# Kernel tuning notes

Hardware: AMD Instinct MI355X
Metric: run time of the kernel (lower is better)

## Reference

```python
import jax, jax.numpy as jnp
import numpy as np

NUM_HEADS = 16
HEAD_DIM = 64  # hidden_size 1024 / 16 heads


def setup_inputs() -> dict:
    key = jax.random.key(0)
    k1, k2, k3, k4 = jax.random.split(key, 4)
    B, S, Dm = 1, 2048, 1024
    scale = 1.0 / np.sqrt(Dm)
    return {
        "hidden_states": jax.random.normal(k1, (B, S, Dm), dtype=jnp.float32),
        "Wq": jax.random.normal(k2, (Dm, Dm), dtype=jnp.float32) * scale,
        "Wk": jax.random.normal(k3, (Dm, Dm), dtype=jnp.float32) * scale,
        "Wv": jax.random.normal(k4, (Dm, Dm), dtype=jnp.float32) * scale,
    }


def reference(hidden_states, Wq, Wk, Wv):
    # hidden_states: [B, S, Dm]; Wq/Wk/Wv: [Dm, Dm] (no bias)
    B, S, Dm = hidden_states.shape
    H, D = NUM_HEADS, HEAD_DIM
    q = (hidden_states @ Wq).reshape(B, S, H, D)
    k = (hidden_states @ Wk).reshape(B, S, H, D)
    v = (hidden_states @ Wv).reshape(B, S, H, D)
    # scaled dot-product scores: [B, H, Sq, Sk]
    scores = jnp.einsum("bqhd,bkhd->bhqk", q, k) / jnp.sqrt(jnp.float32(D))
    probs = jax.nn.softmax(scores, axis=-1)
    # context: [B, Sq, H, D] -> [B, Sq, H*D]
    context = jnp.einsum("bhqk,bkhd->bqhd", probs, v).reshape(B, S, H * D)
    # module permutes scores [B, Sq, Sk, H] -> [B, H, Sq, Sk]; we built that layout directly
    return context, probs
```

## Files before the change

### kernel.cpp

```cpp
#include <hip/hip_runtime.h>
#include <cstdint>
#include <cstddef>

#define SEQ 2048
#define DMODEL 1024
#define NHEADS 16
#define HDIM 64

typedef __attribute__((ext_vector_type(8))) short short8;
typedef __attribute__((ext_vector_type(4))) float floatx4;

__device__ __forceinline__ short f2bf(float f) {
  union { float f; uint32_t u; } x; x.f = f;
  uint32_t r = (x.u + 0x7FFFu + ((x.u >> 16) & 1u)) >> 16;
  return (short)(uint16_t)r;
}

__device__ __forceinline__ void gl_lds16(const short* g, short* l) {
  __builtin_amdgcn_global_load_lds((const __attribute__((address_space(1))) void*)g,
                                   (__attribute__((address_space(3))) void*)l, 16, 0, 0);
}

__global__ __launch_bounds__(256) void cast_bf16_kernel(const float* __restrict__ src,
                                                        short* __restrict__ dst, int n) {
  int i = blockIdx.x * 256 + threadIdx.x;
  if (i < n) dst[i] = f2bf(src[i]);
}

__global__ __launch_bounds__(256) void transpose_cast_kernel(const float* __restrict__ src,
                                                             short* __restrict__ dst) {
  __shared__ float tile[32][33];
  int tx = threadIdx.x, ty = threadIdx.y;
  int x = blockIdx.x * 32 + tx;
  int y0 = blockIdx.y * 32;
#pragma unroll
  for (int j = 0; j < 32; j += 8)
    tile[ty + j][tx] = src[(size_t)(y0 + ty + j) * DMODEL + x];
  __syncthreads();
  int xo = blockIdx.y * 32 + tx;
  int yo0 = blockIdx.x * 32;
#pragma unroll
  for (int j = 0; j < 32; j += 8)
    dst[(size_t)(yo0 + ty + j) * DMODEL + xo] = f2bf(tile[tx][ty + j]);
}

__global__ __launch_bounds__(256) void qkv_gemm_kernel(const short* __restrict__ Xb,
                                                       const short* __restrict__ Wt,
                                                       short* __restrict__ q,
                                                       short* __restrict__ k,
                                                       short* __restrict__ vT) {
  __shared__ short Ab[2][64 * 32];
  __shared__ short Bb[2][128 * 32];
  int tid = threadIdx.x;
  int wave = tid >> 6, lane = tid & 63;
  int lr = lane & 15, quad = lane >> 4;
  int m0 = blockIdx.y * 64;
  int n0 = blockIdx.x * 128;
  int wr = wave >> 1, wc = wave & 1;

  const short* Ag = Xb + (size_t)(m0 + (tid >> 2)) * DMODEL + (tid & 3) * 8;
  const short* Bg = Wt + (size_t)(n0 + (tid >> 2)) * DMODEL + (tid & 3) * 8;
  bool isV = (n0 >= 2 * DMODEL);

  floatx4 acc[2][4] = {};

  gl_lds16(Ag, Ab[0] + wave * 512);
  gl_lds16(Bg, Bb[0] + wave * 512);
  gl_lds16(Bg + 64 * DMODEL, Bb[0] + 2048 + wave * 512);
  __syncthreads();

  int cur = 0;
  for (int t = 0; t < 32; ++t) {
    if (t < 31) {
      int kb = (t + 1) * 32;
      gl_lds16(Ag + kb, Ab[cur ^ 1] + wave * 512);
      gl_lds16(Bg + kb, Bb[cur ^ 1] + wave * 512);
      gl_lds16(Bg + kb + 64 * DMODEL, Bb[cur ^ 1] + 2048 + wave * 512);
    }
    short8 a[2], b[4];
#pragma unroll
    for (int i = 0; i < 2; ++i)
      a[i] = *(const short8*)(Ab[cur] + (wr * 32 + i * 16 + lr) * 32 + quad * 8);
#pragma unroll
    for (int j = 0; j < 4; ++j)
      b[j] = *(const short8*)(Bb[cur] + (wc * 64 + j * 16 + lr) * 32 + quad * 8);
    if (isV) {
#pragma unroll
      for (int i = 0; i < 2; ++i)
#pragma unroll
        for (int j = 0; j < 4; ++j)
          acc[i][j] = __builtin_amdgcn_mfma_f32_16x16x32_bf16(b[j], a[i], acc[i][j], 0, 0, 0);
    } else {
#pragma unroll
      for (int i = 0; i < 2; ++i)
#pragma unroll
        for (int j = 0; j < 4; ++j)
          acc[i][j] = __builtin_amdgcn_mfma_f32_16x16x32_bf16(a[i], b[j], acc[i][j], 0, 0, 0);
    }
    __syncthreads();
    cur ^= 1;
  }

  if (!isV) {
    short* out = (n0 < DMODEL) ? q : k;
    int nbase = n0 & (DMODEL - 1);
#pragma unroll
    for (int i = 0; i < 2; ++i)
#pragma unroll
      for (int j = 0; j < 4; ++j) {
        int n = nbase + wc * 64 + j * 16 + lr;
        int hh = n >> 6, d = n & 63;
        size_t base = ((size_t)hh * SEQ + m0 + wr * 32 + i * 16 + quad * 4) * HDIM + d;
#pragma unroll
        for (int r = 0; r < 4; ++r) out[base + (size_t)r * HDIM] = f2bf(acc[i][j][r]);
      }
  } else {
    int nbase = n0 - 2 * DMODEL;
#pragma unroll
    for (int i = 0; i < 2; ++i) {
      int sidx = m0 + wr * 32 + i * 16 + lr;
#pragma unroll
      for (int j = 0; j < 4; ++j) {
        int n = nbase + wc * 64 + j * 16 + quad * 4;
#pragma unroll
        for (int r = 0; r < 4; ++r) vT[(size_t)(n + r) * SEQ + sidx] = f2bf(acc[i][j][r]);
      }
    }
  }
}

#define PSTRF 132

__global__ __launch_bounds__(256, 4) void attn_fused_kernel(const short* __restrict__ q,
                                                            const short* __restrict__ k,
                                                            const short* __restrict__ vT,
                                                            float* __restrict__ probs,
                                                            float* __restrict__ ctx) {
  __shared__ float pf[4][16 * PSTRF];
  __shared__ float wm[4][16], wl[4][16];

  int h = blockIdx.y;
  int m0 = blockIdx.x * 16;
  int wave = threadIdx.x >> 6, lane = threadIdx.x & 63;
  int lr = lane & 15, quad = lane >> 4;
  int nb = wave * 512;

  const short* Q = q + ((size_t)h * SEQ + m0 + lr) * HDIM + quad * 8;
  short8 qa0 = *(const short8*)(Q);
  short8 qa1 = *(const short8*)(Q + 32);
  const short* K = k + (size_t)h * SEQ * HDIM + quad * 8;

  float mrow[4], lrow[4];
#pragma unroll
  for (int r = 0; r < 4; ++r) { mrow[r] = -3.4e38f; lrow[r] = 0.f; }

#pragma unroll 1
  for (int c = 0; c < 4; ++c) {
    floatx4 s[8];
#pragma unroll
    for (int f = 0; f < 8; ++f) {
      const short* Kr = K + (size_t)(nb + c * 128 + f * 16 + lr) * HDIM;
      short8 b0 = *(const short8*)(Kr);
      short8 b1 = *(const short8*)(Kr + 32);
      floatx4 t = {};
      t = __builtin_amdgcn_mfma_f32_16x16x32_bf16(qa0, b0, t, 0, 0, 0);
      s[f] = __builtin_amdgcn_mfma_f32_16x16x32_bf16(qa1, b1, t, 0, 0, 0);
    }
#pragma unroll
    for (int r = 0; r < 4; ++r) {
      float cm = s[0][r];
#pragma unroll
      for (int f = 1; f < 8; ++f) cm = fmaxf(cm, s[f][r]);
      cm *= 0.125f;
      float mn = fmaxf(mrow[r], cm);
      float sum = 0.f;
#pragma unroll
      for (int f = 0; f < 8; ++f) sum += __expf(s[f][r] * 0.125f - mn);
      lrow[r] = lrow[r] * __expf(mrow[r] - mn) + sum;
      mrow[r] = mn;
    }
  }

#pragma unroll
  for (int off = 8; off >= 1; off >>= 1)
#pragma unroll
    for (int r = 0; r < 4; ++r) {
      float om = __shfl_xor(mrow[r], off);
      float ol = __shfl_xor(lrow[r], off);
      float mn = fmaxf(mrow[r], om);
      lrow[r] = lrow[r] * __expf(mrow[r] - mn) + ol * __expf(om - mn);
      mrow[r] = mn;
    }
  if (lr == 0)
#pragma unroll
    for (int r = 0; r < 4; ++r) {
      wm[wave][quad * 4 + r] = mrow[r];
      wl[wave][quad * 4 + r] = lrow[r];
    }
  __syncthreads();
  float inv[4];
#pragma unroll
  for (int r = 0; r < 4; ++r) {
    int row = quad * 4 + r;
    float m4 = fmaxf(fmaxf(wm[0][row], wm[1][row]), fmaxf(wm[2][row], wm[3][row]));
    float l4 = wl[0][row] * __expf(wm[0][row] - m4) + wl[1][row] * __expf(wm[1][row] - m4) +
               wl[2][row] * __expf(wm[2][row] - m4) + wl[3][row] * __expf(wm[3][row] - m4);
    mrow[r] = m4;
    inv[r] = 1.0f / l4;
  }

  float* pw = pf[wave];
  const short* Vb = vT + (size_t)h * HDIM * SEQ;
  floatx4 cacc[4] = {};
  int prow = lane >> 5;
  int pchunk = lane & 31;

#pragma unroll 1
  for (int c = 0; c < 4; ++c) {
    floatx4 s[8];
#pragma unroll
    for (int f = 0; f < 8; ++f) {
      const short* Kr = K + (size_t)(nb + c * 128 + f * 16 + lr) * HDIM;
      short8 b0 = *(const short8*)(Kr);
      short8 b1 = *(const short8*)(Kr + 32);
      floatx4 t = {};
      t = __builtin_amdgcn_mfma_f32_16x16x32_bf16(qa0, b0, t, 0, 0, 0);
      s[f] = __builtin_amdgcn_mfma_f32_16x16x32_bf16(qa1, b1, t, 0, 0, 0);
    }
#pragma unroll
    for (int f = 0; f < 8; ++f)
#pragma unroll
      for (int r = 0; r < 4; ++r)
        pw[(quad * 4 + r) * PSTRF + f * 16 + lr] = __expf(s[f][r] * 0.125f - mrow[r]) * inv[r];
#pragma unroll
    for (int i = 0; i < 8; ++i) {
      int row = i * 2 + prow;
      floatx4 v4 = *(const floatx4*)(pw + row * PSTRF + pchunk * 4);
      __builtin_nontemporal_store(
          v4, (floatx4*)(probs + ((size_t)h * SEQ + m0 + row) * SEQ + nb + c * 128 + pchunk * 4));
    }
#pragma unroll
    for (int kt = 0; kt < 128; kt += 32) {
      const float* pa = pw + lr * PSTRF + kt + quad * 8;
      floatx4 p0 = *(const floatx4*)(pa);
      floatx4 p1 = *(const floatx4*)(pa + 4);
      short8 a;
#pragma unroll
      for (int j = 0; j < 4; ++j) {
        a[j] = f2bf(p0[j]);
        a[4 + j] = f2bf(p1[j]);
      }
#pragma unroll
      for (int f = 0; f < 4; ++f) {
        short8 b = *(const short8*)(Vb + (size_t)(f * 16 + lr) * SEQ + nb + c * 128 + kt + quad * 8);
        cacc[f] = __builtin_amdgcn_mfma_f32_16x16x32_bf16(a, b, cacc[f], 0, 0, 0);
      }
    }
  }

  float* part = pf[wave];
#pragma unroll
  for (int f = 0; f < 4; ++f)
#pragma unroll
    for (int r = 0; r < 4; ++r) part[(quad * 4 + r) * 64 + f * 16 + lr] = cacc[f][r];
  __syncthreads();
  for (int e = threadIdx.x; e < 16 * 64; e += 256) {
    int m = e >> 6, d = e & 63;
    float v = pf[0][m * 64 + d] + pf[1][m * 64 + d] + pf[2][m * 64 + d] + pf[3][m * 64 + d];
    ctx[(size_t)(m0 + m) * DMODEL + h * HDIM + d] = v;
  }
}

extern "C" void kernel_launch(void* const* d_in, const int* in_sizes, int n_in,
                              void* d_out, int out_size, void* d_ws, size_t ws_size,
                              hipStream_t stream) {
  const float* X = (const float*)d_in[0];
  const float* Wq = (const float*)d_in[1];
  const float* Wk = (const float*)d_in[2];
  const float* Wv = (const float*)d_in[3];

  float* ctx = (float*)d_out;
  float* probs = (float*)d_out + (size_t)SEQ * DMODEL;

  short* Xb = (short*)d_ws;
  short* Wt = Xb + (size_t)SEQ * DMODEL;
  short* qb = Wt + (size_t)3 * DMODEL * DMODEL;
  short* kb = qb + (size_t)NHEADS * SEQ * HDIM;
  short* vT = kb + (size_t)NHEADS * SEQ * HDIM;

  cast_bf16_kernel<<<(SEQ * DMODEL + 255) / 256, 256, 0, stream>>>(X, Xb, SEQ * DMODEL);
  dim3 tb(32, 8), tg(32, 32);
  transpose_cast_kernel<<<tg, tb, 0, stream>>>(Wq, Wt);
  transpose_cast_kernel<<<tg, tb, 0, stream>>>(Wk, Wt + (size_t)DMODEL * DMODEL);
  transpose_cast_kernel<<<tg, tb, 0, stream>>>(Wv, Wt + (size_t)2 * DMODEL * DMODEL);

  qkv_gemm_kernel<<<dim3(3 * DMODEL / 128, SEQ / 64), 256, 0, stream>>>(Xb, Wt, qb, kb, vT);
  attn_fused_kernel<<<dim3(SEQ / 16, NHEADS), 256, 0, stream>>>(qb, kb, vT, probs, ctx);
}
```

Measured before the change: 453.0 us.

## Split attention into context kernel and separate probs-writing kernel

The fused attention kernel no longer writes the probability matrix. It stores per-row max and inverse sum to workspace. A new probs kernel recomputes QK^T, applies the saved softmax statistics, and writes probs with software-pipelined stores: the previous chunk's stores are issued while the next K tiles load. The aim is to decouple the large probs write stream from the PV compute so each kernel can be scheduled better, at the cost of recomputing QK^T and an extra launch. Probs stores also change from nontemporal to ordinary stores.

```diff
diff --git a/kernel.cpp b/kernel.cpp
--- a/kernel.cpp
+++ b/kernel.cpp
@@ -131,11 +131,12 @@
 
 #define PSTRF 132
 
-__global__ __launch_bounds__(256, 4) void attn_fused_kernel(const short* __restrict__ q,
-                                                            const short* __restrict__ k,
-                                                            const short* __restrict__ vT,
-                                                            float* __restrict__ probs,
-                                                            float* __restrict__ ctx) {
+__global__ __launch_bounds__(256, 4) void attn_ctx_kernel(const short* __restrict__ q,
+                                                          const short* __restrict__ k,
+                                                          const short* __restrict__ vT,
+                                                          float* __restrict__ smx,
+                                                          float* __restrict__ six,
+                                                          float* __restrict__ ctx) {
   __shared__ float pf[4][16 * PSTRF];
   __shared__ float wm[4][16], wl[4][16];
 
@@ -208,12 +209,16 @@
     mrow[r] = m4;
     inv[r] = 1.0f / l4;
   }
+  if (wave == 0 && lr == 0)
+#pragma unroll
+    for (int r = 0; r < 4; ++r) {
+      smx[(size_t)h * SEQ + m0 + quad * 4 + r] = mrow[r];
+      six[(size_t)h * SEQ + m0 + quad * 4 + r] = inv[r];
+    }
 
   float* pw = pf[wave];
   const short* Vb = vT + (size_t)h * HDIM * SEQ;
   floatx4 cacc[4] = {};
-  int prow = lane >> 5;
-  int pchunk = lane & 31;
 
 #pragma unroll 1
   for (int c = 0; c < 4; ++c) {
@@ -233,13 +238,6 @@
       for (int r = 0; r < 4; ++r)
         pw[(quad * 4 + r) * PSTRF + f * 16 + lr] = __expf(s[f][r] * 0.125f - mrow[r]) * inv[r];
 #pragma unroll
-    for (int i = 0; i < 8; ++i) {
-      int row = i * 2 + prow;
-      floatx4 v4 = *(const floatx4*)(pw + row * PSTRF + pchunk * 4);
-      __builtin_nontemporal_store(
-          v4, (floatx4*)(probs + ((size_t)h * SEQ + m0 + row) * SEQ + nb + c * 128 + pchunk * 4));
-    }
-#pragma unroll
     for (int kt = 0; kt < 128; kt += 32) {
       const float* pa = pw + lr * PSTRF + kt + quad * 8;
       floatx4 p0 = *(const floatx4*)(pa);
@@ -268,6 +266,75 @@
     int m = e >> 6, d = e & 63;
     float v = pf[0][m * 64 + d] + pf[1][m * 64 + d] + pf[2][m * 64 + d] + pf[3][m * 64 + d];
     ctx[(size_t)(m0 + m) * DMODEL + h * HDIM + d] = v;
+  }
+}
+
+__global__ __launch_bounds__(256) void probs_kernel(const short* __restrict__ q,
+                                                    const short* __restrict__ k,
+                                                    const float* __restrict__ smx,
+                                                    const float* __restrict__ six,
+                                                    float* __restrict__ probs) {
+  __shared__ float pf[4][16 * PSTRF];
+
+  int h = blockIdx.y;
+  int m0 = blockIdx.x * 16;
+  int wave = threadIdx.x >> 6, lane = threadIdx.x & 63;
+  int lr = lane & 15, quad = lane >> 4;
+  int nb = wave * 512;
+
+  const short* Q = q + ((size_t)h * SEQ + m0 + lr) * HDIM + quad * 8;
+  short8 qa0 = *(const short8*)(Q);
+  short8 qa1 = *(const short8*)(Q + 32);
+  const short* K = k + (size_t)h * SEQ * HDIM + quad * 8;
+
+  float mr[4], inv[4];
+#pragma unroll
+  for (int r = 0; r < 4; ++r) {
+    mr[r] = smx[(size_t)h * SEQ + m0 + quad * 4 + r];
+    inv[r] = six[(size_t)h * SEQ + m0 + quad * 4 + r];
+  }
+
+  float* pw = pf[wave];
+  int prow = lane >> 5, pchunk = lane & 31;
+  floatx4 hold[8];
+  float* Pg0 = probs + ((size_t)h * SEQ + m0) * SEQ + nb;
+
+#pragma unroll 1
+  for (int c = 0; c < 4; ++c) {
+    short8 kb0[8], kb1[8];
+#pragma unroll
+    for (int f = 0; f < 8; ++f) {
+      const short* Kr = K + (size_t)(nb + c * 128 + f * 16 + lr) * HDIM;
+      kb0[f] = *(const short8*)(Kr);
+      kb1[f] = *(const short8*)(Kr + 32);
+    }
+    if (c > 0) {
+#pragma unroll
+      for (int i = 0; i < 8; ++i) {
+        int row = i * 2 + prow;
+        *(floatx4*)(Pg0 + (size_t)row * SEQ + (c - 1) * 128 + pchunk * 4) = hold[i];
+      }
+    }
+    floatx4 s[8];
+#pragma unroll
+    for (int f = 0; f < 8; ++f) {
+      floatx4 t = {};
+      t = __builtin_amdgcn_mfma_f32_16x16x32_bf16(qa0, kb0[f], t, 0, 0, 0);
+      s[f] = __builtin_amdgcn_mfma_f32_16x16x32_bf16(qa1, kb1[f], t, 0, 0, 0);
+    }
+#pragma unroll
+    for (int f = 0; f < 8; ++f)
+#pragma unroll
+      for (int r = 0; r < 4; ++r)
+        pw[(quad * 4 + r) * PSTRF + f * 16 + lr] = __expf(s[f][r] * 0.125f - mr[r]) * inv[r];
+#pragma unroll
+    for (int i = 0; i < 8; ++i)
+      hold[i] = *(const floatx4*)(pw + (i * 2 + prow) * PSTRF + pchunk * 4);
+  }
+#pragma unroll
+  for (int i = 0; i < 8; ++i) {
+    int row = i * 2 + prow;
+    *(floatx4*)(Pg0 + (size_t)row * SEQ + 3 * 128 + pchunk * 4) = hold[i];
   }
 }
 
@@ -287,6 +354,8 @@
   short* qb = Wt + (size_t)3 * DMODEL * DMODEL;
   short* kb = qb + (size_t)NHEADS * SEQ * HDIM;
   short* vT = kb + (size_t)NHEADS * SEQ * HDIM;
+  float* smx = (float*)(vT + (size_t)NHEADS * HDIM * SEQ);
+  float* six = smx + (size_t)NHEADS * SEQ;
 
   cast_bf16_kernel<<<(SEQ * DMODEL + 255) / 256, 256, 0, stream>>>(X, Xb, SEQ * DMODEL);
   dim3 tb(32, 8), tg(32, 32);
@@ -295,5 +364,6 @@
   transpose_cast_kernel<<<tg, tb, 0, stream>>>(Wv, Wt + (size_t)2 * DMODEL * DMODEL);
 
   qkv_gemm_kernel<<<dim3(3 * DMODEL / 128, SEQ / 64), 256, 0, stream>>>(Xb, Wt, qb, kb, vT);
-  attn_fused_kernel<<<dim3(SEQ / 16, NHEADS), 256, 0, stream>>>(qb, kb, vT, probs, ctx);
-}
+  attn_ctx_kernel<<<dim3(SEQ / 16, NHEADS), 256, 0, stream>>>(qb, kb, vT, smx, six, ctx);
+  probs_kernel<<<dim3(SEQ / 16, NHEADS), 256, 0, stream>>>(qb, kb, smx, six, probs);
+}
```

New measurement: 524.1 us. 15.7% more time.
